# Performance work log

Hardware: AMD Instinct MI355X
Metric: run time of the kernel (lower is better)

## Reference

```python
import jax, jax.numpy as jnp
import numpy as np

DG = 8            # deformable_groups
MAX_RES = 10.0    # max_residual_magnitude
K = 9             # 3x3 kernel positions


def conv3(x, w, b):
    y = jax.lax.conv_general_dilated(x, w, (1, 1), [(1, 1), (1, 1)],
                                     dimension_numbers=('NCHW', 'OIHW', 'NCHW'))
    return y + b[None, :, None, None]


def lrelu(v):
    return jnp.where(v >= 0, v, 0.1 * v)


def deform_conv2d(x, offset, mask, weight, bias):
    # x: [B,C,H,W]; offset: [B,2*DG*K,H,W] (per group, K points, (y,x) interleaved)
    # mask: [B,DG*K,H,W]; weight: [O,C,3,3]; stride=1, pad=1, dil=1, groups=1
    B, C, H, W = x.shape
    Cg = C // DG
    off = offset.reshape(B, DG, K, 2, H, W)
    dtype = x.dtype
    dy = (jnp.arange(K) // 3 - 1).astype(dtype)
    dx = (jnp.arange(K) % 3 - 1).astype(dtype)
    py = off[:, :, :, 0] + jnp.arange(H, dtype=dtype)[None, None, None, :, None] + dy[None, None, :, None, None]
    px = off[:, :, :, 1] + jnp.arange(W, dtype=dtype)[None, None, None, None, :] + dx[None, None, :, None, None]
    y0 = jnp.floor(py)
    x0 = jnp.floor(px)
    x_flat = x.reshape(B, DG, Cg, H * W)
    m = mask.reshape(B, DG, K, H, W)
    acc = jnp.zeros((B, DG, Cg, K, H, W), dtype=dtype)
    for iy, wy in ((y0, y0 + 1.0 - py), (y0 + 1.0, py - y0)):
        for ix, wx in ((x0, x0 + 1.0 - px), (x0 + 1.0, px - x0)):
            valid = (iy >= 0) & (iy < H) & (ix >= 0) & (ix < W)
            yi = jnp.clip(iy, 0, H - 1).astype(jnp.int32)
            xi = jnp.clip(ix, 0, W - 1).astype(jnp.int32)
            idx = (yi * W + xi).reshape(B, DG, 1, K * H * W)
            g = jnp.take_along_axis(x_flat, idx, axis=3).reshape(B, DG, Cg, K, H, W)
            wgt = (wy * wx * valid.astype(dtype) * m)[:, :, None]  # mask folded in
            acc = acc + g * wgt
    O = weight.shape[0]
    out = jnp.einsum('bgckhw,ogck->bohw', acc, weight.reshape(O, DG, Cg, K))
    return out + bias[None, :, None, None]


def setup_inputs() -> dict:
    key = jax.random.key(0)
    ks = jax.random.split(key, 12)
    B, C, H, W = 4, 64, 128, 128
    inp = {
        'x': jax.random.normal(ks[0], (B, C, H, W), jnp.float32),
        'x_warped0': jax.random.normal(ks[1], (B, C, H, W), jnp.float32),
        'x_current': jax.random.normal(ks[2], (B, C, H, W), jnp.float32),
        'flow0': jax.random.normal(ks[3], (B, 2, H, W), jnp.float32),
        'w1': jax.random.normal(ks[4], (64, 130, 3, 3), jnp.float32) * 0.05,
        'b1': jnp.zeros((64,), jnp.float32),
        'w2': jax.random.normal(ks[5], (64, 64, 3, 3), jnp.float32) * 0.05,
        'b2': jnp.zeros((64,), jnp.float32),
        'w3': jax.random.normal(ks[6], (64, 64, 3, 3), jnp.float32) * 0.05,
        'b3': jnp.zeros((64,), jnp.float32),
        'w4': jax.random.normal(ks[7], (216, 64, 3, 3), jnp.float32) * 0.05,
        'b4': jnp.zeros((216,), jnp.float32),
        'weight': jax.random.normal(ks[8], (64, 64, 3, 3), jnp.float32) * 0.05,
        'bias': jnp.zeros((64,), jnp.float32),
    }
    return inp


def reference(x, x_warped0, x_current, flow0, w1, b1, w2, b2, w3, b3, w4, b4, weight, bias):
    # conv_offset stack on cat([x_warped0, x_current, flow0])
    feat = jnp.concatenate([x_warped0, x_current, flow0], axis=1)  # [B, 2C+2, H, W]
    o = lrelu(conv3(feat, w1, b1))
    o = lrelu(conv3(o, w2, b2))
    o = lrelu(conv3(o, w3, b3))
    o = conv3(o, w4, b4)  # [B, 3*K*DG, H, W]
    out1, out2, mask = jnp.split(o, 3, axis=1)
    offset = MAX_RES * jnp.tanh(jnp.concatenate([out1, out2], axis=1))  # [B, 2*K*DG, H, W]
    # flows[0].flip(1).repeat(1, K*DG, 1, 1): (y,x) flow tiled over all sample points
    offset = offset + jnp.tile(flow0[:, ::-1], (1, K * DG, 1, 1))
    mask = jax.nn.sigmoid(mask)
    return deform_conv2d(x, offset, mask, weight, bias)
```

## Files before the change

### kernel.cpp

```cpp
#include <hip/hip_runtime.h>
#include <math.h>

#define HH 128
#define WW 128
#define BB 4
#define HW (HH*WW)

typedef unsigned short u16;
typedef unsigned int u32;
typedef __bf16 bf16x8 __attribute__((ext_vector_type(8)));
typedef float f32x4 __attribute__((ext_vector_type(4)));

__device__ __forceinline__ u16 f2bf(float x) {
    u32 u = __float_as_uint(x);
    return (u16)((u + 0x7fffu + ((u >> 16) & 1u)) >> 16);
}
__device__ __forceinline__ float bf2f(u16 h) {
    return __uint_as_float(((u32)h) << 16);
}
__device__ __forceinline__ bf16x8 ld8(const u16* p) {
    union { uint4 u; bf16x8 v; } c;
    c.u = *(const uint4*)p;
    return c.v;
}
__device__ __forceinline__ bf16x8 cvt8(uint4 u) {
    union { uint4 u; bf16x8 v; } c;
    c.u = u;
    return c.v;
}

__global__ void split_w_k(const float* __restrict__ src, u16* __restrict__ dh,
                          u16* __restrict__ dl, int OC, int OCpad, int CIN, int CINpad)
{
    const int i = blockIdx.x * 256 + threadIdx.x;
    const int tot = OCpad * 9 * CINpad;
    if (i >= tot) return;
    const int oc = i / (9 * CINpad);
    const int r = i - oc * 9 * CINpad;
    const int tap = r / CINpad;
    const int cin = r - tap * CINpad;
    float v = 0.f;
    if (oc < OC && cin < CIN) v = src[((size_t)oc * CIN + cin) * 9 + tap];
    const u16 h = f2bf(v);
    dh[i] = h;
    dl[i] = f2bf(v - bf2f(h));
}

__global__ void pad_bias_k(const float* __restrict__ b, float* __restrict__ bp)
{
    const int i = blockIdx.x * 256 + threadIdx.x;
    if (i < 256) bp[i] = (i < 216) ? b[i] : 0.f;
}

__global__ void pack_dw_k(const float* __restrict__ wt, u16* __restrict__ Apack)
{
    const int i = blockIdx.x * 256 + threadIdx.x;
    if (i >= 36864) return;
    const int jj = i & 7;
    const int fr = (i >> 3) & 15;
    const int m  = (i >> 7) & 3;
    const int fq = (i >> 9) & 3;
    const int kk = i >> 11;
    const int oc = m * 16 + fr;
    const int j  = kk * 32 + fq * 8 + jj;
    const int tap = j >> 3, c = j & 7;
    const int g = tap / 9, kt = tap - g * 9;
    const int ch = g * 8 + c;
    Apack[i] = f2bf(wt[((size_t)oc * 64 + ch) * 9 + kt]);
}

template<int CREC>
__global__ __launch_bounds__(256) void pack_x_k(
    const float* __restrict__ A, const float* __restrict__ B2,
    const float* __restrict__ C3, u16* __restrict__ dst)
{
    const int i = blockIdx.x * 256 + threadIdx.x;
    const int b = i >> 14;
    const int px = i & 16383;
    u16* rec = dst + (size_t)i * (CREC * 2);

#pragma unroll
    for (int g = 0; g < CREC / 32; ++g) {
#pragma unroll
        for (int cb = 0; cb < 4; ++cb) {
            u32 hwv[4], lwv[4];
#pragma unroll
            for (int p = 0; p < 4; ++p) {
                float v[2];
#pragma unroll
                for (int e = 0; e < 2; ++e) {
                    const int c = g * 32 + cb * 8 + p * 2 + e;
                    float vv;
                    if (c < 64)       vv = A[((size_t)(b * 64 + c)) * HW + px];
                    else if (c < 128) vv = B2[((size_t)(b * 64 + c - 64)) * HW + px];
                    else if (c < 130) vv = C3[((size_t)(b * 2 + c - 128)) * HW + px];
                    else              vv = 0.f;
                    v[e] = vv;
                }
                const u16 h0 = f2bf(v[0]), h1 = f2bf(v[1]);
                const u16 l0 = f2bf(v[0] - bf2f(h0)), l1 = f2bf(v[1] - bf2f(h1));
                hwv[p] = (u32)h0 | ((u32)h1 << 16);
                lwv[p] = (u32)l0 | ((u32)l1 << 16);
            }
            uint4 H; H.x = hwv[0]; H.y = hwv[1]; H.z = hwv[2]; H.w = hwv[3];
            uint4 L; L.x = lwv[0]; L.y = lwv[1]; L.z = lwv[2]; L.w = lwv[3];
            *(uint4*)(rec + g * 64 + cb * 16)     = H;
            *(uint4*)(rec + g * 64 + cb * 16 + 8) = L;
        }
    }
}

template<int NCHUNK, int KGLAST, int MODE, bool RELU, bool PACKOUT, int MINW, int NJ>
__global__ __launch_bounds__(256, MINW) void conv_pk_k(
    const u16* __restrict__ Xp, const u16* __restrict__ Wh, const u16* __restrict__ Wl,
    const float* __restrict__ bias, float* __restrict__ outf, u16* __restrict__ outp,
    int OCreal, int mtile0)
{
    const int ROWS = (MODE == 1) ? 8 : 4;
    const int NPX = (ROWS + 2) * 18;
    __shared__ u16 Xs[NPX * 136];
    const int CINpad = (NCHUNK - 1) * 64 + KGLAST * 32;
    const int CRECU16 = CINpad * 2;

    const int tile = blockIdx.x;
    const int h0 = (tile >> 3) * ROWS;
    const int w0 = (tile & 7) * 16;
    const int b = blockIdx.z;
    const int t = threadIdx.x;
    const int lane = t & 63, wv = t >> 6;
    const int fr = lane & 15, fq = lane >> 4;

    const int mg = wv >> 1, rg = wv & 1;
    const int mbase = (MODE == 1) ? (mtile0 + mg * NJ) : 0;

    f32x4 acc0[4];
    f32x4 acc1[NJ][4];
    if (MODE == 0) {
        const float4 bv = *(const float4*)(bias + wv * 16 + 4 * fq);
#pragma unroll
        for (int n = 0; n < 4; ++n) {
            acc0[n][0] = bv.x; acc0[n][1] = bv.y; acc0[n][2] = bv.z; acc0[n][3] = bv.w;
        }
    } else {
#pragma unroll
        for (int m = 0; m < NJ; ++m) {
            const float4 bv = *(const float4*)(bias + (mbase + m) * 16 + 4 * fq);
#pragma unroll
            for (int n = 0; n < 4; ++n) {
                acc1[m][n][0] = bv.x; acc1[m][n][1] = bv.y;
                acc1[m][n][2] = bv.z; acc1[m][n][3] = bv.w;
            }
        }
    }

    const u16* WhL = Wh + (size_t)fr * 9 * CINpad + 8 * fq;
    const u16* WlL = Wl + (size_t)fr * 9 * CINpad + 8 * fq;

#pragma unroll
    for (int chunk = 0; chunk < NCHUNK; ++chunk) {
        const int nkg = (chunk == NCHUNK - 1) ? KGLAST : 2;
        const int nu = nkg * 8;
        __syncthreads();
        for (int s = t; s < NPX * nu; s += 256) {
            const int px = s / nu, o = s - px * nu;
            const int hy = px / 18, hx = px - hy * 18;
            const int gy = h0 + hy - 1, gx = w0 + hx - 1;
            uint4 v; v.x = 0; v.y = 0; v.z = 0; v.w = 0;
            if (gy >= 0 && gy < HH && gx >= 0 && gx < WW)
                v = *(const uint4*)(Xp + ((size_t)(b * HW + gy * WW + gx)) * CRECU16
                                       + chunk * 128 + o * 8);
            *(uint4*)(Xs + px * 136 + o * 8) = v;
        }
        __syncthreads();

        if (MODE == 0) {
#pragma unroll
            for (int tap = 0; tap < 9; ++tap) {
                const int ky = tap / 3, kx = tap % 3;
#pragma unroll
                for (int kg = 0; kg < 2; ++kg) {
                    if (kg >= nkg) break;
                    const size_t off = (size_t)(wv * 144 + tap) * CINpad + chunk * 64 + kg * 32;
                    const bf16x8 Ah = ld8(WhL + off);
                    const bf16x8 Al = ld8(WlL + off);
#pragma unroll
                    for (int n = 0; n < 4; ++n) {
                        const int hp = (n + ky) * 18 + fr + kx;
                        const u16* Bp = Xs + hp * 136 + kg * 64 + fq * 16;
                        const bf16x8 Bh = ld8(Bp);
                        const bf16x8 Bl = ld8(Bp + 8);
                        acc0[n] = __builtin_amdgcn_mfma_f32_16x16x32_bf16(Ah, Bh, acc0[n], 0, 0, 0);
                        acc0[n] = __builtin_amdgcn_mfma_f32_16x16x32_bf16(Ah, Bl, acc0[n], 0, 0, 0);
                        acc0[n] = __builtin_amdgcn_mfma_f32_16x16x32_bf16(Al, Bh, acc0[n], 0, 0, 0);
                    }
                }
            }
        } else {
            auto PF = [&](int tap, bf16x8 (&Dh)[2 * NJ], bf16x8 (&Dl)[2 * NJ]) {
#pragma unroll
                for (int kg = 0; kg < 2; ++kg)
#pragma unroll
                    for (int m = 0; m < NJ; ++m) {
                        const size_t off = (size_t)((mbase + m) * 144 + tap) * CINpad
                                         + chunk * 64 + kg * 32;
                        Dh[kg * NJ + m] = ld8(WhL + off);
                        Dl[kg * NJ + m] = ld8(WlL + off);
                    }
            };
            auto CMP = [&](int tap, bf16x8 (&Dh)[2 * NJ], bf16x8 (&Dl)[2 * NJ]) {
                const int ky = tap / 3, kx = tap - 3 * ky;
#pragma unroll
                for (int kg = 0; kg < 2; ++kg) {
#pragma unroll
                    for (int n = 0; n < 4; ++n) {
                        const int hp = (rg * 4 + n + ky) * 18 + fr + kx;
                        const u16* Bp = Xs + hp * 136 + kg * 64 + fq * 16;
                        const bf16x8 Bh = ld8(Bp);
                        const bf16x8 Bl = ld8(Bp + 8);
#pragma unroll
                        for (int m = 0; m < NJ; ++m) {
                            acc1[m][n] = __builtin_amdgcn_mfma_f32_16x16x32_bf16(Dh[kg * NJ + m], Bh, acc1[m][n], 0, 0, 0);
                            acc1[m][n] = __builtin_amdgcn_mfma_f32_16x16x32_bf16(Dh[kg * NJ + m], Bl, acc1[m][n], 0, 0, 0);
                            acc1[m][n] = __builtin_amdgcn_mfma_f32_16x16x32_bf16(Dl[kg * NJ + m], Bh, acc1[m][n], 0, 0, 0);
                        }
                    }
                }
            };

            bf16x8 PaH[2 * NJ], PaL[2 * NJ], PbH[2 * NJ], PbL[2 * NJ];
            PF(0, PaH, PaL);
#pragma unroll 1
            for (int tp = 0; tp < 4; ++tp) {
                PF(2 * tp + 1, PbH, PbL);
                CMP(2 * tp, PaH, PaL);
                PF(2 * tp + 2, PaH, PaL);
                CMP(2 * tp + 1, PbH, PbL);
            }
            CMP(8, PaH, PaL);
        }
    }

    if (MODE == 1) {
#pragma unroll
        for (int m = 0; m < NJ; ++m)
#pragma unroll
            for (int n = 0; n < 4; ++n)
#pragma unroll
                for (int i = 0; i < 4; ++i) {
                    const int oc = (mbase + m) * 16 + 4 * fq + i;
                    if (oc < OCreal) {
                        float v = acc1[m][n][i];
                        if (RELU) v = (v >= 0.f) ? v : 0.1f * v;
                        outf[((size_t)(b * OCreal + oc)) * HW + (h0 + rg * 4 + n) * WW + w0 + fr] = v;
                    }
                }
    } else if (!PACKOUT) {
#pragma unroll
        for (int n = 0; n < 4; ++n)
#pragma unroll
            for (int i = 0; i < 4; ++i) {
                const int oc = wv * 16 + 4 * fq + i;
                if (oc < OCreal) {
                    float v = acc0[n][i];
                    if (RELU) v = (v >= 0.f) ? v : 0.1f * v;
                    outf[((size_t)(b * OCreal + oc)) * HW + (h0 + n) * WW + w0 + fr] = v;
                }
            }
    } else {
        __syncthreads();
        const int coff = (wv >> 1) * 64 + (((wv << 1) + (fq >> 1)) & 3) * 16 + ((fq & 1) << 2);
#pragma unroll
        for (int n = 0; n < 4; ++n) {
            u16 hh[4], ll[4];
#pragma unroll
            for (int i = 0; i < 4; ++i) {
                float v = acc0[n][i];
                if (RELU) v = (v >= 0.f) ? v : 0.1f * v;
                hh[i] = f2bf(v);
                ll[i] = f2bf(v - bf2f(hh[i]));
            }
            uint2 H, L;
            H.x = (u32)hh[0] | ((u32)hh[1] << 16);
            H.y = (u32)hh[2] | ((u32)hh[3] << 16);
            L.x = (u32)ll[0] | ((u32)ll[1] << 16);
            L.y = (u32)ll[2] | ((u32)ll[3] << 16);
            const int pxe = n * 16 + fr;
            u16* E = Xs + pxe * 136 + coff;
            *(uint2*)E = H;
            *(uint2*)(E + 8) = L;
        }
        __syncthreads();
        for (int i = t; i < 1024; i += 256) {
            const int px = i >> 4, o = i & 15;
            const uint4 v = *(const uint4*)(Xs + px * 136 + o * 8);
            const int gp = (h0 + (px >> 4)) * WW + w0 + (px & 15);
            *(uint4*)(outp + ((size_t)(b * HW + gp)) * 128 + o * 8) = v;
        }
    }
}

__global__ __launch_bounds__(256) void pack_xb_k(
    const float* __restrict__ x, uint4* __restrict__ xqb)
{
    const int i = blockIdx.x * 256 + threadIdx.x;
    const int pix = i & (HW - 1);
    const int g = (i >> 14) & 7;
    const int b = i >> 17;
    const float* xp = x + ((size_t)(b * 64 + g * 8)) * HW + pix;
    u32 w[4];
#pragma unroll
    for (int c2 = 0; c2 < 4; ++c2) {
        const u16 l = f2bf(xp[(size_t)(2 * c2) * HW]);
        const u16 h = f2bf(xp[(size_t)(2 * c2 + 1) * HW]);
        w[c2] = (u32)l | ((u32)h << 16);
    }
    uint4 v; v.x = w[0]; v.y = w[1]; v.z = w[2]; v.w = w[3];
    xqb[(size_t)(b * 8 + g) * HW + pix] = v;
}

__device__ __forceinline__ unsigned pk_bf16(float lo, float hi) {
    unsigned a = __float_as_uint(lo), b = __float_as_uint(hi);
    return ((a + 0x8000u) >> 16) | ((b + 0x8000u) & 0xffff0000u);
}

__global__ __launch_bounds__(512, 8) void deform_fused_k(
    const uint4* __restrict__ xqb, const float* __restrict__ o4,
    const float* __restrict__ flow, const uint4* __restrict__ Apack,
    const float* __restrict__ bias, float* __restrict__ out)
{
    __shared__ u16 sv[32 * 584];

    const int bid0 = blockIdx.x;
    const int bid = (bid0 & 7) * 256 + (bid0 >> 3);
    const int b = bid >> 9;
    const int pix0 = (bid & 511) << 5;
    const int t = threadIdx.x;

    {
        const int gpx = t & 31;
        const int g = (t >> 5) & 7;
        const int kh = t >> 8;
        const int kbase = kh * 4;
        const int pix = pix0 + gpx;
        const int h = pix >> 7, w = pix & (WW - 1);
        const float fy = flow[((size_t)b * 2 + 1) * HW + pix];
        const float fx = flow[((size_t)b * 2 + 0) * HW + pix];
        const float* ob = o4 + (size_t)b * 216 * HW + pix;
        const uint4* qg = xqb + (size_t)(b * 8 + g) * HW;

        int   code[5];
        float w00[5], w01[5], w10[5], w11[5];

#pragma unroll
        for (int j = 0; j < 5; ++j) {
            if (j == 4 && !kh) break;
            const int k = kbase + j;
            const float oy = ob[(size_t)(g * 18 + k * 2) * HW];
            const float ox = ob[(size_t)(g * 18 + k * 2 + 1) * HW];
            float mm = ob[(size_t)(144 + g * 9 + k) * HW];
            mm = __builtin_amdgcn_rcpf(1.f + __expf(-mm));

            const float ay = fabsf(oy), ax = fabsf(ox);
            const float ey = __expf(-2.f * ay), ex = __expf(-2.f * ax);
            float ty = (1.f - ey) * __builtin_amdgcn_rcpf(1.f + ey);
            float tx = (1.f - ex) * __builtin_amdgcn_rcpf(1.f + ex);
            ty = copysignf(ty, oy); tx = copysignf(tx, ox);

            const float ppy = 10.f * ty + fy + (float)(h + k / 3 - 1);
            const float ppx = 10.f * tx + fx + (float)(w + k % 3 - 1);

            const float y0f = floorf(ppy), x0f = floorf(ppx);
            const float ly = ppy - y0f, lx = ppx - x0f;
            const int iy0 = (int)y0f, ix0 = (int)x0f;
            const int iy1 = iy0 + 1,  ix1 = ix0 + 1;

            const float vy0 = (iy0 >= 0 && iy0 < HH) ? 1.f : 0.f;
            const float vy1 = (iy1 >= 0 && iy1 < HH) ? 1.f : 0.f;
            const float vx0 = (ix0 >= 0 && ix0 < WW) ? 1.f : 0.f;
            const float vx1 = (ix1 >= 0 && ix1 < WW) ? 1.f : 0.f;

            const int cy0 = min(max(iy0, 0), HH - 1);
            const int cy1 = min(max(iy1, 0), HH - 1);
            const int cx0 = min(max(ix0, 0), WW - 1);
            const int cx1 = min(max(ix1, 0), WW - 1);

            w00[j] = (1.f - ly) * (1.f - lx) * vy0 * vx0 * mm;
            w01[j] = (1.f - ly) * lx         * vy0 * vx1 * mm;
            w10[j] = ly         * (1.f - lx) * vy1 * vx0 * mm;
            w11[j] = ly         * lx         * vy1 * vx1 * mm;

            code[j] = (cy0 * WW + cx0) | ((cx1 - cx0) << 14) | ((cy1 - cy0) << 15);
        }

        u16* svp = sv + gpx * 584 + g * 72 + kbase * 8;
#pragma unroll
        for (int j = 0; j < 5; ++j) {
            if (j == 4 && !kh) break;
            const int i00 = code[j] & 16383;
            const int i01 = i00 + ((code[j] >> 14) & 1);
            const int i10 = i00 + (((code[j] >> 15) & 1) << 7);
            const int i11 = i10 + ((code[j] >> 14) & 1);

            const uint4 A4 = qg[i00];
            const uint4 B4 = qg[i01];
            const uint4 C4 = qg[i10];
            const uint4 D4 = qg[i11];
            const float W00 = w00[j], W01 = w01[j], W10 = w10[j], W11 = w11[j];

            uint4 P;
            u32 pw[4];
#pragma unroll
            for (int c2 = 0; c2 < 4; ++c2) {
                const u32 aw = (&A4.x)[c2], bw = (&B4.x)[c2];
                const u32 cw = (&C4.x)[c2], dw = (&D4.x)[c2];
                const float alo = __uint_as_float(aw << 16), ahi = __uint_as_float(aw & 0xffff0000u);
                const float blo = __uint_as_float(bw << 16), bhi = __uint_as_float(bw & 0xffff0000u);
                const float clo = __uint_as_float(cw << 16), chi = __uint_as_float(cw & 0xffff0000u);
                const float dlo = __uint_as_float(dw << 16), dhi = __uint_as_float(dw & 0xffff0000u);
                const float slo = W00 * alo + W01 * blo + W10 * clo + W11 * dlo;
                const float shi = W00 * ahi + W01 * bhi + W10 * chi + W11 * dhi;
                pw[c2] = pk_bf16(slo, shi);
            }
            P.x = pw[0]; P.y = pw[1]; P.z = pw[2]; P.w = pw[3];
            *(uint4*)(svp + (size_t)j * 8) = P;
        }
    }
    __syncthreads();

    {
        const int lane = t & 63, wv = t >> 6;
        const int mt = wv & 3, nt = wv >> 2;
        const int fr = lane & 15, fq = lane >> 4;

        f32x4 acc;
        acc[0] = 0.f; acc[1] = 0.f; acc[2] = 0.f; acc[3] = 0.f;

#pragma unroll
        for (int kk = 0; kk < 18; ++kk) {
            const bf16x8 A = cvt8(Apack[((kk * 4 + fq) * 4 + mt) * 16 + fr]);
            const bf16x8 Bf = ld8(sv + (size_t)(nt * 16 + fr) * 584 + kk * 32 + fq * 8);
            acc = __builtin_amdgcn_mfma_f32_16x16x32_bf16(A, Bf, acc, 0, 0, 0);
        }

        const float4 bv = *(const float4*)(bias + mt * 16 + 4 * fq);
        const float bb[4] = { bv.x, bv.y, bv.z, bv.w };
        const int pix = pix0 + nt * 16 + fr;
#pragma unroll
        for (int i = 0; i < 4; ++i) {
            const int oc = mt * 16 + 4 * fq + i;
            out[((size_t)b * 64 + oc) * HW + pix] = acc[i] + bb[i];
        }
    }
}

extern "C" void kernel_launch(void* const* d_in, const int* in_sizes, int n_in,
                              void* d_out, int out_size, void* d_ws, size_t ws_size,
                              hipStream_t stream)
{
    const float* x     = (const float*)d_in[0];
    const float* xw    = (const float*)d_in[1];
    const float* xc    = (const float*)d_in[2];
    const float* flow  = (const float*)d_in[3];
    const float* w1    = (const float*)d_in[4];
    const float* b1    = (const float*)d_in[5];
    const float* w2    = (const float*)d_in[6];
    const float* b2    = (const float*)d_in[7];
    const float* w3    = (const float*)d_in[8];
    const float* b3    = (const float*)d_in[9];
    const float* w4    = (const float*)d_in[10];
    const float* b4    = (const float*)d_in[11];
    const float* wt    = (const float*)d_in[12];
    const float* bias  = (const float*)d_in[13];
    float* out = (float*)d_out;

    char* ws = (char*)d_ws;
    u16*   X1p  = (u16*)(ws);
    float* o4   = (float*)(ws);
    u16*   buf1 = (u16*)(ws + 56623104);
    u16*   buf2 = (u16*)(ws + 73400320);
    u16* Apack = (u16*)(ws + 90177536);
    u16* W1h = (u16*)(ws + 90251264);
    u16* W1l = (u16*)(ws + 90435584);
    u16* W2h = (u16*)(ws + 90619904);
    u16* W2l = (u16*)(ws + 90693632);
    u16* W3h = (u16*)(ws + 90767360);
    u16* W3l = (u16*)(ws + 90841088);
    u16* W4h = (u16*)(ws + 90914816);
    u16* W4l = (u16*)(ws + 91209728);
    float* b4p = (float*)(ws + 91504640);

    const dim3 blk(256);

    split_w_k<<<dim3((64 * 9 * 160 + 255) / 256), blk, 0, stream>>>(w1, W1h, W1l, 64, 64, 130, 160);
    split_w_k<<<dim3((64 * 9 * 64 + 255) / 256), blk, 0, stream>>>(w2, W2h, W2l, 64, 64, 64, 64);
    split_w_k<<<dim3((64 * 9 * 64 + 255) / 256), blk, 0, stream>>>(w3, W3h, W3l, 64, 64, 64, 64);
    split_w_k<<<dim3((256 * 9 * 64 + 255) / 256), blk, 0, stream>>>(w4, W4h, W4l, 216, 256, 64, 64);
    pad_bias_k<<<dim3(1), blk, 0, stream>>>(b4, b4p);
    pack_dw_k<<<dim3(144), blk, 0, stream>>>(wt, Apack);

    pack_x_k<160><<<dim3(BB * HW / 256), blk, 0, stream>>>(xw, xc, flow, X1p);
    conv_pk_k<3, 1, 0, true, true, 2, 4><<<dim3(256, 1, BB), blk, 0, stream>>>(
        X1p, W1h, W1l, b1, nullptr, buf1, 64, 0);
    conv_pk_k<1, 2, 0, true, true, 2, 4><<<dim3(256, 1, BB), blk, 0, stream>>>(
        buf1, W2h, W2l, b2, nullptr, buf2, 64, 0);
    conv_pk_k<1, 2, 0, true, true, 2, 4><<<dim3(256, 1, BB), blk, 0, stream>>>(
        buf2, W3h, W3l, b3, nullptr, buf1, 64, 0);
    pack_xb_k<<<dim3(BB * 8 * HW / 256), blk, 0, stream>>>(x, (uint4*)buf2);
    conv_pk_k<1, 2, 1, false, false, 1, 4><<<dim3(128, 1, BB), blk, 0, stream>>>(
        buf1, W4h, W4l, b4p, o4, nullptr, 216, 0);
    conv_pk_k<1, 2, 1, false, false, 1, 3><<<dim3(128, 1, BB), blk, 0, stream>>>(
        buf1, W4h, W4l, b4p, o4, nullptr, 216, 8);

    deform_fused_k<<<dim3(BB * HW / 32), dim3(512), 0, stream>>>(
        (const uint4*)buf2, o4, flow, (const uint4*)Apack, bias, out);
}
```

Before: 280.1 us.

## Fuse tanh/sigmoid into conv4 epilogue and merge conv4 launches

Applies the offset tanh scaling and mask sigmoid in the conv4 output epilogue instead of recomputing them in the deform kernel. The two conv4 launches that split output-channel tiles are merged into one launch with 4-row pixel tiles, where each wave owns 4 channel tiles. This removes redundant transcendental work and a launch, but weight reuse across the two row groups of the old 8-row tile is lost.

```diff
diff --git a/kernel.cpp b/kernel.cpp
--- a/kernel.cpp
+++ b/kernel.cpp
@@ -114,9 +114,9 @@
 __global__ __launch_bounds__(256, MINW) void conv_pk_k(
     const u16* __restrict__ Xp, const u16* __restrict__ Wh, const u16* __restrict__ Wl,
     const float* __restrict__ bias, float* __restrict__ outf, u16* __restrict__ outp,
-    int OCreal, int mtile0)
-{
-    const int ROWS = (MODE == 1) ? 8 : 4;
+    int OCreal)
+{
+    const int ROWS = 4;
     const int NPX = (ROWS + 2) * 18;
     __shared__ u16 Xs[NPX * 136];
     const int CINpad = (NCHUNK - 1) * 64 + KGLAST * 32;
@@ -130,8 +130,7 @@
     const int lane = t & 63, wv = t >> 6;
     const int fr = lane & 15, fq = lane >> 4;
 
-    const int mg = wv >> 1, rg = wv & 1;
-    const int mbase = (MODE == 1) ? (mtile0 + mg * NJ) : 0;
+    const int mbase = (MODE == 1) ? (wv * NJ) : 0;
 
     f32x4 acc0[4];
     f32x4 acc1[NJ][4];
@@ -213,7 +212,7 @@
                 for (int kg = 0; kg < 2; ++kg) {
 #pragma unroll
                     for (int n = 0; n < 4; ++n) {
-                        const int hp = (rg * 4 + n + ky) * 18 + fr + kx;
+                        const int hp = (n + ky) * 18 + fr + kx;
                         const u16* Bp = Xs + hp * 136 + kg * 64 + fq * 16;
                         const bf16x8 Bh = ld8(Bp);
                         const bf16x8 Bl = ld8(Bp + 8);
@@ -242,18 +241,27 @@
 
     if (MODE == 1) {
 #pragma unroll
-        for (int m = 0; m < NJ; ++m)
+        for (int m = 0; m < NJ; ++m) {
+            const int mt = mbase + m;
 #pragma unroll
             for (int n = 0; n < 4; ++n)
 #pragma unroll
                 for (int i = 0; i < 4; ++i) {
-                    const int oc = (mbase + m) * 16 + 4 * fq + i;
+                    const int oc = mt * 16 + 4 * fq + i;
                     if (oc < OCreal) {
                         float v = acc1[m][n][i];
-                        if (RELU) v = (v >= 0.f) ? v : 0.1f * v;
-                        outf[((size_t)(b * OCreal + oc)) * HW + (h0 + rg * 4 + n) * WW + w0 + fr] = v;
+                        if (mt < 9) {
+                            const float a = fabsf(v);
+                            const float e = __expf(-2.f * a);
+                            float tv = (1.f - e) * __builtin_amdgcn_rcpf(1.f + e);
+                            v = 10.f * copysignf(tv, v);
+                        } else {
+                            v = __builtin_amdgcn_rcpf(1.f + __expf(-v));
+                        }
+                        outf[((size_t)(b * OCreal + oc)) * HW + (h0 + n) * WW + w0 + fr] = v;
                     }
                 }
+        }
     } else if (!PACKOUT) {
 #pragma unroll
         for (int n = 0; n < 4; ++n)
@@ -357,17 +365,10 @@
             const int k = kbase + j;
             const float oy = ob[(size_t)(g * 18 + k * 2) * HW];
             const float ox = ob[(size_t)(g * 18 + k * 2 + 1) * HW];
-            float mm = ob[(size_t)(144 + g * 9 + k) * HW];
-            mm = __builtin_amdgcn_rcpf(1.f + __expf(-mm));
-
-            const float ay = fabsf(oy), ax = fabsf(ox);
-            const float ey = __expf(-2.f * ay), ex = __expf(-2.f * ax);
-            float ty = (1.f - ey) * __builtin_amdgcn_rcpf(1.f + ey);
-            float tx = (1.f - ex) * __builtin_amdgcn_rcpf(1.f + ex);
-            ty = copysignf(ty, oy); tx = copysignf(tx, ox);
-
-            const float ppy = 10.f * ty + fy + (float)(h + k / 3 - 1);
-            const float ppx = 10.f * tx + fx + (float)(w + k % 3 - 1);
+            const float mm = ob[(size_t)(144 + g * 9 + k) * HW];
+
+            const float ppy = oy + fy + (float)(h + k / 3 - 1);
+            const float ppx = ox + fx + (float)(w + k % 3 - 1);
 
             const float y0f = floorf(ppy), x0f = floorf(ppx);
             const float ly = ppy - y0f, lx = ppx - x0f;
@@ -500,16 +501,14 @@
 
     pack_x_k<160><<<dim3(BB * HW / 256), blk, 0, stream>>>(xw, xc, flow, X1p);
     conv_pk_k<3, 1, 0, true, true, 2, 4><<<dim3(256, 1, BB), blk, 0, stream>>>(
-        X1p, W1h, W1l, b1, nullptr, buf1, 64, 0);
+        X1p, W1h, W1l, b1, nullptr, buf1, 64);
     conv_pk_k<1, 2, 0, true, true, 2, 4><<<dim3(256, 1, BB), blk, 0, stream>>>(
-        buf1, W2h, W2l, b2, nullptr, buf2, 64, 0);
+        buf1, W2h, W2l, b2, nullptr, buf2, 64);
     conv_pk_k<1, 2, 0, true, true, 2, 4><<<dim3(256, 1, BB), blk, 0, stream>>>(
-        buf2, W3h, W3l, b3, nullptr, buf1, 64, 0);
+        buf2, W3h, W3l, b3, nullptr, buf1, 64);
     pack_xb_k<<<dim3(BB * 8 * HW / 256), blk, 0, stream>>>(x, (uint4*)buf2);
-    conv_pk_k<1, 2, 1, false, false, 1, 4><<<dim3(128, 1, BB), blk, 0, stream>>>(
-        buf1, W4h, W4l, b4p, o4, nullptr, 216, 0);
-    conv_pk_k<1, 2, 1, false, false, 1, 3><<<dim3(128, 1, BB), blk, 0, stream>>>(
-        buf1, W4h, W4l, b4p, o4, nullptr, 216, 8);
+    conv_pk_k<1, 2, 1, false, false, 1, 4><<<dim3(256, 1, BB), blk, 0, stream>>>(
+        buf1, W4h, W4l, b4p, o4, nullptr, 216);
 
     deform_fused_k<<<dim3(BB * HW / 32), dim3(512), 0, stream>>>(
         (const uint4*)buf2, o4, flow, (const uint4*)Apack, bias, out);
```

Result: no change. 285.4 us (+1.9%).
